# Kernel tuning notes

Measured on AMD Instinct MI355X. Metric: run time of the kernel, lower is better.

## Reference

```python
import jax, jax.numpy as jnp
import numpy as np

IMG_H, IMG_W = 800.0, 1280.0
STRIDE = 16
SCALE = 1.0 / STRIDE
P, S = 14, 1              # pooler resolution, sampling ratio
NUM_CLASSES = 80
BBOX_W = (10.0, 10.0, 5.0, 5.0)
SCORE_TH, NMS_TH, MAX_DET, IOU_TH = 0.05, 0.5, 100, 0.5
SCALE_CLAMP = float(np.log(1000.0 / 16.0))


def _make_boxes(key, n_img, n_box):
    k1, k2, k3, k4 = jax.random.split(key, 4)
    x1 = jax.random.uniform(k1, (n_img, n_box)) * (IMG_W - 64.0)
    y1 = jax.random.uniform(k2, (n_img, n_box)) * (IMG_H - 64.0)
    w = jax.random.uniform(k3, (n_img, n_box)) * 300.0 + 16.0
    h = jax.random.uniform(k4, (n_img, n_box)) * 300.0 + 16.0
    x2 = jnp.minimum(x1 + w, IMG_W)
    y2 = jnp.minimum(y1 + h, IMG_H)
    return jnp.stack([x1, y1, x2, y2], axis=-1)


def setup_inputs() -> dict:
    key = jax.random.key(0)
    ks = jax.random.split(key, 6)
    features = jax.random.normal(ks[0], (2, 50, 80, 1024), dtype=jnp.float32)
    proposals = _make_boxes(ks[1], 2, 256)
    gt_boxes = _make_boxes(ks[2], 2, 64)
    gt_classes = jax.random.randint(ks[3], (2, 64), 0, NUM_CLASSES)
    W_cls = jax.random.normal(ks[4], (1024, NUM_CLASSES + 1), dtype=jnp.float32) * 0.01
    b_cls = jnp.zeros((NUM_CLASSES + 1,), jnp.float32)
    W_box = jax.random.normal(ks[5], (1024, 4), dtype=jnp.float32) * 0.01
    b_box = jnp.zeros((4,), jnp.float32)
    return {"features": features, "proposals": proposals, "gt_boxes": gt_boxes,
            "gt_classes": gt_classes, "W_cls": W_cls, "b_cls": b_cls,
            "W_box": W_box, "b_box": b_box}


def pairwise_iou(a, b):
    # a: [G,4], b: [R,4], boxes as (x1,y1,x2,y2) -> [G,R]
    area_a = (a[:, 2] - a[:, 0]) * (a[:, 3] - a[:, 1])
    area_b = (b[:, 2] - b[:, 0]) * (b[:, 3] - b[:, 1])
    lt = jnp.maximum(a[:, None, :2], b[None, :, :2])
    rb = jnp.minimum(a[:, None, 2:], b[None, :, 2:])
    wh = jnp.clip(rb - lt, 0.0)
    inter = wh[..., 0] * wh[..., 1]
    return inter / jnp.maximum(area_a[:, None] + area_b[None, :] - inter, 1e-9)


def roi_align_one(feat, boxes):
    # feat: [H,W,C], boxes: [R,4] in image coords -> pooled [R,P,P,C]
    H, W, C = feat.shape
    b = boxes * SCALE
    x1, y1, x2, y2 = b[:, 0], b[:, 1], b[:, 2], b[:, 3]
    off = (jnp.arange(S, dtype=feat.dtype) + 0.5) / S       # [S]
    grid = jnp.arange(P, dtype=feat.dtype)                   # [P]
    bh = ((y2 - y1) / P)[:, None, None]
    bw = ((x2 - x1) / P)[:, None, None]
    # aligned RoIAlign sample coords (half-pixel offset)
    gy = y1[:, None, None] + (grid[None, :, None] + off[None, None, :]) * bh - 0.5  # [R,P,S]
    gx = x1[:, None, None] + (grid[None, :, None] + off[None, None, :]) * bw - 0.5
    gy = jnp.clip(gy, 0.0, H - 1.0)
    gx = jnp.clip(gx, 0.0, W - 1.0)
    y0 = jnp.floor(gy); x0 = jnp.floor(gx)
    y0i = y0.astype(jnp.int32); x0i = x0.astype(jnp.int32)
    y1i = jnp.minimum(y0i + 1, H - 1); x1i = jnp.minimum(x0i + 1, W - 1)
    ly = gy - y0; lx = gx - x0

    def g(yi, xi):  # cross-product gather -> [R,P,S,P,S,C]
        return feat[yi[:, :, :, None, None], xi[:, None, None, :, :]]

    wy0 = (1.0 - ly)[:, :, :, None, None, None]; wy1 = ly[:, :, :, None, None, None]
    wx0 = (1.0 - lx)[:, None, None, :, :, None]; wx1 = lx[:, None, None, :, :, None]
    val = wy0 * (wx0 * g(y0i, x0i) + wx1 * g(y0i, x1i)) \
        + wy1 * (wx0 * g(y1i, x0i) + wx1 * g(y1i, x1i))
    return val.mean(axis=(2, 4))  # average sampling points per bin -> [R,P,P,C]


def decode_boxes(deltas, boxes):
    wx, wy, ww, wh = BBOX_W
    widths = boxes[..., 2] - boxes[..., 0]
    heights = boxes[..., 3] - boxes[..., 1]
    ctr_x = boxes[..., 0] + 0.5 * widths
    ctr_y = boxes[..., 1] + 0.5 * heights
    dx = deltas[..., 0] / wx
    dy = deltas[..., 1] / wy
    dw = jnp.minimum(deltas[..., 2] / ww, SCALE_CLAMP)
    dh = jnp.minimum(deltas[..., 3] / wh, SCALE_CLAMP)
    pcx = dx * widths + ctr_x
    pcy = dy * heights + ctr_y
    pw = jnp.exp(dw) * widths
    ph = jnp.exp(dh) * heights
    out = jnp.stack([pcx - 0.5 * pw, pcy - 0.5 * ph, pcx + 0.5 * pw, pcy + 0.5 * ph], axis=-1)
    lim = jnp.array([IMG_W, IMG_H, IMG_W, IMG_H], out.dtype)
    return jnp.clip(out, 0.0, lim)


def nms_keep(boxes, scores):
    # greedy class-agnostic NMS, fixed-size keep mask [R]
    R = scores.shape[0]
    order = jnp.argsort(-scores)
    sb = boxes[order]
    iou = pairwise_iou(sb, sb)
    idx = jnp.arange(R)

    def body(i, keep):
        suppressed = jnp.any((idx < i) & keep & (iou[:, i] > NMS_TH))
        return keep.at[i].set(jnp.logical_not(suppressed))

    keep_sorted = jax.lax.fori_loop(0, R, body, jnp.ones((R,), bool))
    return jnp.zeros((R,), bool).at[order].set(keep_sorted)


def reference(features, proposals, gt_boxes, gt_classes, W_cls, b_cls, W_box, b_box):
    N, R = proposals.shape[:2]
    # --- proposal <-> gt matching (training-side labeling) ---
    iou_m = jax.vmap(pairwise_iou)(gt_boxes, proposals)          # [N,G,R]
    matched_vals = iou_m.max(axis=1)
    matched_idxs = iou_m.argmax(axis=1)                          # [N,R]
    match_labels = (matched_vals >= IOU_TH).astype(jnp.int32)    # [N,R] fg=1/bg=0
    # --- RoIAlign pooling on the single C4 feature map ---
    pooled = jax.vmap(roi_align_one)(features, proposals)        # [N,R,P,P,C]
    feat_vec = pooled.mean(axis=(2, 3))                          # res5 surrogate global avg -> [N,R,C]
    # --- box predictor ---
    scores_all = jax.nn.softmax(feat_vec @ W_cls + b_cls, axis=-1)
    fg_scores = scores_all[..., :NUM_CLASSES].max(axis=-1)       # drop background column
    deltas = feat_vec @ W_box + b_box
    boxes = decode_boxes(deltas, proposals)                      # [N,R,4]
    # --- score threshold + NMS + top-k ---
    keep = jax.vmap(nms_keep)(boxes, fg_scores) & (fg_scores > SCORE_TH)
    masked = jnp.where(keep, fg_scores, -jnp.inf)
    rank = jnp.argsort(jnp.argsort(-masked, axis=-1), axis=-1)
    keep = keep & (rank < MAX_DET)
    det = jnp.concatenate([boxes, fg_scores[..., None], keep.astype(boxes.dtype)[..., None]], axis=-1)
    return det, matched_idxs, match_labels
```

## Files before the change

kernel.cpp:

```cpp
#include <hip/hip_runtime.h>
#include <math.h>

#define N_IMG 2
#define R_PROP 256
#define G_GT 64
#define C_CH 1024
#define FH 50
#define FW 80
#define P_POOL 14
#define NCLS 80
#define IMG_W_F 1280.0f
#define IMG_H_F 800.0f
#define SCALE_F 0.0625f
#define SCORE_TH_F 0.05f
#define NMS_TH_F 0.5f
#define IOU_TH_F 0.5f
#define MAX_DET_I 100
#define SCALE_CLAMP_F 4.135166556742356f

#define NQ 4
#define QCH (C_CH / NQ)

__global__ __launch_bounds__(512) void prep_kernel(
    const float* __restrict__ proposals,
    const float* __restrict__ gt_boxes,
    int* __restrict__ perm,
    float* __restrict__ out_idx,
    float* __restrict__ out_lbl) {
  const int t = threadIdx.x;
  const int n = t >> 8;
  __shared__ float cy[N_IMG * R_PROP];
  const float* pb = proposals + (size_t)t * 4;
  float bx1 = pb[0], by1 = pb[1], bx2 = pb[2], by2 = pb[3];
  cy[t] = by1 + by2;
  __syncthreads();

  {
    float my = cy[t];
    int rk = 0;
    const int base = n * R_PROP;
#pragma unroll 8
    for (int j = base; j < base + R_PROP; ++j) {
      float cj = cy[j];
      rk += (cj < my) || (cj == my && j < t);
    }
    perm[base + rk] = t & 255;
  }

  {
    float area_b = (bx2 - bx1) * (by2 - by1);
    float best = -1.0f;
    int bidx = 0;
    const float* gt = gt_boxes + (size_t)n * G_GT * 4;
#pragma unroll 4
    for (int g = 0; g < G_GT; ++g) {
      float gx1 = gt[g * 4 + 0], gy1 = gt[g * 4 + 1];
      float gx2 = gt[g * 4 + 2], gy2 = gt[g * 4 + 3];
      float area_a = (gx2 - gx1) * (gy2 - gy1);
      float ix1 = fmaxf(gx1, bx1), iy1 = fmaxf(gy1, by1);
      float ix2 = fminf(gx2, bx2), iy2 = fminf(gy2, by2);
      float iw = fmaxf(ix2 - ix1, 0.0f), ih = fmaxf(iy2 - iy1, 0.0f);
      float inter = iw * ih;
      float iou = inter / fmaxf(area_a + area_b - inter, 1e-9f);
      if (iou > best) { best = iou; bidx = g; }
    }
    out_idx[t] = (float)bidx;
    out_lbl[t] = (best >= IOU_TH_F) ? 1.0f : 0.0f;
  }
}

__global__ __launch_bounds__(256) void roihead_kernel(
    const float* __restrict__ features,
    const float* __restrict__ proposals,
    const int* __restrict__ perm,
    const float* __restrict__ W_cls,
    const float* __restrict__ W_box,
    float* __restrict__ part) {
  const int b = blockIdx.x;
  const int xcd = b & 7;
  const int slot = b >> 3;
  const int n = xcd >> 2;
  const int band = xcd & 3;
  const int q = slot & 3;
  const int p = n * R_PROP + perm[n * R_PROP + band * 64 + (slot >> 2)];
  const int qbase = q * QCH;

  const float* feat = features + (size_t)n * (FH * FW * C_CH) + qbase;
  const int t = threadIdx.x;
  const int c4 = t & 63;
  const int g = t >> 6;

  __shared__ float s_Wy[FH];
  __shared__ float s_Wx[FW];
  __shared__ int s_b[4];
  __shared__ float4 s_red[3][64];
  __shared__ __align__(16) float sf[QCH];
  __shared__ float s_part[3][85];

  if (t < FH) s_Wy[t] = 0.0f;
  if (t >= 128 && t < 128 + FW) s_Wx[t - 128] = 0.0f;
  __syncthreads();

  if (t < 2 * P_POOL) {
    const float* pb = proposals + (size_t)p * 4;
    bool isY = t < P_POOL;
    int i = isY ? t : t - P_POOL;
    float lo = isY ? pb[1] : pb[0];
    float hi = isY ? pb[3] : pb[2];
    float limit = isY ? (float)(FH - 1) : (float)(FW - 1);
    float b1 = lo * SCALE_F, b2 = hi * SCALE_F;
    float bs = (b2 - b1) * (1.0f / P_POOL);
    float gg = b1 + ((float)i + 0.5f) * bs - 0.5f;
    gg = fminf(fmaxf(gg, 0.0f), limit);
    float fl = floorf(gg);
    int i0 = (int)fl;
    int i1 = min(i0 + 1, (int)limit);
    float l = gg - fl;
    if (isY) {
      atomicAdd(&s_Wy[i0], 1.0f - l);
      atomicAdd(&s_Wy[i1], l);
      if (i == 0) s_b[0] = i0;
      if (i == P_POOL - 1) s_b[1] = i1;
    } else {
      atomicAdd(&s_Wx[i0], 1.0f - l);
      atomicAdd(&s_Wx[i1], l);
      if (i == 0) s_b[2] = i0;
      if (i == P_POOL - 1) s_b[3] = i1;
    }
  }
  __syncthreads();

  {
    const int ylo = s_b[0], yhi = s_b[1], xlo = s_b[2], xhi = s_b[3];
    float4 acc = make_float4(0.f, 0.f, 0.f, 0.f);
    for (int y = ylo + g; y <= yhi; y += 4) {
      float wy = s_Wy[y];
      const float4* row = (const float4*)(feat + (size_t)y * (FW * C_CH)) + c4;
#pragma unroll 8
      for (int x = xlo; x <= xhi; ++x) {
        float w = wy * s_Wx[x];
        float4 f = row[x * (C_CH / 4)];
        acc.x += w * f.x;
        acc.y += w * f.y;
        acc.z += w * f.z;
        acc.w += w * f.w;
      }
    }
    if (g > 0) s_red[g - 1][c4] = acc;
    __syncthreads();
    if (g == 0) {
      const float inv = 1.0f / (float)(P_POOL * P_POOL);
#pragma unroll
      for (int r = 0; r < 3; ++r) {
        float4 a = s_red[r][c4];
        acc.x += a.x; acc.y += a.y; acc.z += a.z; acc.w += a.w;
      }
      ((float4*)sf)[c4] =
          make_float4(acc.x * inv, acc.y * inv, acc.z * inv, acc.w * inv);
    }
    __syncthreads();
  }

  {
    const int kq = t / 85;
    const int j = t - kq * 85;
    if (kq < 3) {
      float acc = 0.0f;
      if (j < 81) {
        const float* __restrict__ w = W_cls + (size_t)qbase * 81 + j;
#pragma unroll 8
        for (int k = kq; k < QCH; k += 3) acc += sf[k] * w[k * 81];
      } else {
        const float* __restrict__ w = W_box + (size_t)qbase * 4 + (j - 81);
#pragma unroll 8
        for (int k = kq; k < QCH; k += 3) acc += sf[k] * w[k * 4];
      }
      s_part[kq][j] = acc;
    }
  }
  __syncthreads();

  if (t < 85) {
    float acc = s_part[0][t] + s_part[1][t] + s_part[2][t];
    part[((size_t)p * NQ + q) * 85 + t] = acc;
  }
}

__global__ __launch_bounds__(128) void finalize_kernel(
    const float* __restrict__ part,
    const float* __restrict__ proposals,
    const float* __restrict__ b_cls,
    const float* __restrict__ b_box,
    float* __restrict__ boxes_dec,
    float* __restrict__ scores) {
  const int blk = blockIdx.x;
  const int t = threadIdx.x;
  __shared__ float sl[85];
  __shared__ float s_red[8];

  const float* pp = part + (size_t)blk * (NQ * 85);
  if (t < 85) {
    float bias = (t < 81) ? b_cls[t] : b_box[t - 81];
    sl[t] = pp[t] + pp[85 + t] + pp[170 + t] + pp[255 + t] + bias;
  }
  __syncthreads();

  {
    float xm = (t < 81) ? sl[t] : -INFINITY;
    float xf = (t < NCLS) ? sl[t] : -INFINITY;
#pragma unroll
    for (int off = 32; off; off >>= 1) {
      xm = fmaxf(xm, __shfl_down(xm, off, 64));
      xf = fmaxf(xf, __shfl_down(xf, off, 64));
    }
    if ((t & 63) == 0) { s_red[t >> 6] = xm; s_red[2 + (t >> 6)] = xf; }
  }
  __syncthreads();
  const float m = fmaxf(s_red[0], s_red[1]);
  {
    float xs = (t < 81) ? expf(sl[t] - m) : 0.0f;
#pragma unroll
    for (int off = 32; off; off >>= 1) xs += __shfl_down(xs, off, 64);
    if ((t & 63) == 0) s_red[4 + (t >> 6)] = xs;
  }
  __syncthreads();

  if (t == 0) {
    float sum = s_red[4] + s_red[5];
    float fgm = fmaxf(s_red[2], s_red[3]);
    scores[blk] = expf(fgm - m) / sum;

    const float* pb = proposals + (size_t)blk * 4;
    float w = pb[2] - pb[0], h = pb[3] - pb[1];
    float cx = pb[0] + 0.5f * w, cy = pb[1] + 0.5f * h;
    float dx = sl[81] * 0.1f;
    float dy = sl[82] * 0.1f;
    float dw = fminf(sl[83] * 0.2f, SCALE_CLAMP_F);
    float dh = fminf(sl[84] * 0.2f, SCALE_CLAMP_F);
    float pcx = dx * w + cx, pcy = dy * h + cy;
    float pw = expf(dw) * w, ph = expf(dh) * h;
    float ox1 = fminf(fmaxf(pcx - 0.5f * pw, 0.0f), IMG_W_F);
    float oy1 = fminf(fmaxf(pcy - 0.5f * ph, 0.0f), IMG_H_F);
    float ox2 = fminf(fmaxf(pcx + 0.5f * pw, 0.0f), IMG_W_F);
    float oy2 = fminf(fmaxf(pcy + 0.5f * ph, 0.0f), IMG_H_F);
    float* bd = boxes_dec + (size_t)blk * 4;
    bd[0] = ox1; bd[1] = oy1; bd[2] = ox2; bd[3] = oy2;
  }
}

__global__ __launch_bounds__(1024) void nms_kernel(
    const float* __restrict__ boxes_dec,
    const float* __restrict__ scores,
    float* __restrict__ det) {
  const int n = blockIdx.x;
  const int u = threadIdx.x;
  const int i = u & 255;
  const int q = u >> 8;
  const int j40 = q * 16;

  __shared__ __align__(16) float ss[R_PROP];
  __shared__ float4 sbs[R_PROP];
  __shared__ int s_part[4 * R_PROP];
  __shared__ int s_rank[R_PROP];
  __shared__ __align__(16) unsigned long long s_mask[R_PROP * 4];
  __shared__ unsigned long long s_keep[4];
  __shared__ __align__(16) float sm[R_PROP];

  float4 myb;
  float mys;
  if (q == 0) {
    myb = ((const float4*)boxes_dec)[n * R_PROP + i];
    mys = scores[n * R_PROP + i];
    ss[i] = mys;
  }
  __syncthreads();

  {
    float s = ss[i];
    int cnt = 0;
#pragma unroll
    for (int j4 = j40; j4 < j40 + 16; ++j4) {
      float4 v = ((const float4*)ss)[j4];
      int jb = j4 * 4;
      cnt += (v.x > s) || (v.x == s && jb + 0 < i);
      cnt += (v.y > s) || (v.y == s && jb + 1 < i);
      cnt += (v.z > s) || (v.z == s && jb + 2 < i);
      cnt += (v.w > s) || (v.w == s && jb + 3 < i);
    }
    s_part[q * R_PROP + i] = cnt;
  }
  __syncthreads();
  if (q == 0) {
    int rk = s_part[i] + s_part[R_PROP + i] + s_part[2 * R_PROP + i] +
             s_part[3 * R_PROP + i];
    s_rank[i] = rk;
    sbs[rk] = myb;
  }
  __syncthreads();

  {
    float4 bi = sbs[i];
    float area_i = (bi.z - bi.x) * (bi.w - bi.y);
    unsigned long long m = 0;
    const int j0 = q * 64;
#pragma unroll 8
    for (int jj = 0; jj < 64; ++jj) {
      float4 bj = sbs[j0 + jj];
      float area_j = (bj.z - bj.x) * (bj.w - bj.y);
      float ix1 = fmaxf(bi.x, bj.x), iy1 = fmaxf(bi.y, bj.y);
      float ix2 = fminf(bi.z, bj.z), iy2 = fminf(bi.w, bj.w);
      float iw = fmaxf(ix2 - ix1, 0.0f), ih = fmaxf(iy2 - iy1, 0.0f);
      float inter = iw * ih;
      float iou = inter / fmaxf(area_i + area_j - inter, 1e-9f);
      m |= (iou > NMS_TH_F) ? (1ull << jj) : 0ull;
    }
    s_mask[i * 4 + q] = m;
  }
  __syncthreads();

  if (u == 0) {
    unsigned long long K0 = ~0ull, K1 = ~0ull, K2 = ~0ull, K3 = ~0ull;
#pragma unroll 16
    for (int b = 1; b < 64; ++b) {
      unsigned long long m0 = s_mask[(size_t)b * 4 + 0];
      unsigned long long sup = m0 & K0 & ((1ull << b) - 1ull);
      K0 = sup ? (K0 & ~(1ull << b)) : K0;
    }
#pragma unroll 16
    for (int b = 0; b < 64; ++b) {
      const unsigned long long* mi = &s_mask[(size_t)(64 + b) * 4];
      unsigned long long m0 = mi[0], m1 = mi[1];
      unsigned long long sup = (m0 & K0) | (m1 & K1 & ((1ull << b) - 1ull));
      K1 = sup ? (K1 & ~(1ull << b)) : K1;
    }
#pragma unroll 16
    for (int b = 0; b < 64; ++b) {
      const unsigned long long* mi = &s_mask[(size_t)(128 + b) * 4];
      unsigned long long m0 = mi[0], m1 = mi[1], m2 = mi[2];
      unsigned long long sup =
          (m0 & K0) | (m1 & K1) | (m2 & K2 & ((1ull << b) - 1ull));
      K2 = sup ? (K2 & ~(1ull << b)) : K2;
    }
#pragma unroll 16
    for (int b = 0; b < 64; ++b) {
      const unsigned long long* mi = &s_mask[(size_t)(192 + b) * 4];
      unsigned long long m0 = mi[0], m1 = mi[1], m2 = mi[2], m3 = mi[3];
      unsigned long long sup = (m0 & K0) | (m1 & K1) | (m2 & K2) |
                               (m3 & K3 & ((1ull << b) - 1ull));
      K3 = sup ? (K3 & ~(1ull << b)) : K3;
    }
    s_keep[0] = K0; s_keep[1] = K1; s_keep[2] = K2; s_keep[3] = K3;
  }
  __syncthreads();

  bool kept = false;
  if (q == 0) {
    int rk = s_rank[i];
    kept = ((s_keep[rk >> 6] >> (rk & 63)) & 1ull) && (mys > SCORE_TH_F);
    sm[i] = kept ? mys : -INFINITY;
  }
  __syncthreads();

  {
    float mym = sm[i];
    int cnt = 0;
#pragma unroll
    for (int j4 = j40; j4 < j40 + 16; ++j4) {
      float4 v = ((const float4*)sm)[j4];
      int jb = j4 * 4;
      cnt += (v.x > mym) || (v.x == mym && jb + 0 < i);
      cnt += (v.y > mym) || (v.y == mym && jb + 1 < i);
      cnt += (v.z > mym) || (v.z == mym && jb + 2 < i);
      cnt += (v.w > mym) || (v.w == mym && jb + 3 < i);
    }
    s_part[q * R_PROP + i] = cnt;
  }
  __syncthreads();

  if (q == 0) {
    int rk2 = s_part[i] + s_part[R_PROP + i] + s_part[2 * R_PROP + i] +
              s_part[3 * R_PROP + i];
    kept = kept && (rk2 < MAX_DET_I);
    float* dr = det + ((size_t)n * R_PROP + i) * 6;
    dr[0] = myb.x; dr[1] = myb.y; dr[2] = myb.z; dr[3] = myb.w;
    dr[4] = mys;
    dr[5] = kept ? 1.0f : 0.0f;
  }
}

extern "C" void kernel_launch(void* const* d_in, const int* in_sizes, int n_in,
                              void* d_out, int out_size, void* d_ws, size_t ws_size,
                              hipStream_t stream) {
  const float* features  = (const float*)d_in[0];
  const float* proposals = (const float*)d_in[1];
  const float* gt_boxes  = (const float*)d_in[2];
  const float* W_cls = (const float*)d_in[4];
  const float* b_cls = (const float*)d_in[5];
  const float* W_box = (const float*)d_in[6];
  const float* b_box = (const float*)d_in[7];

  float* out = (float*)d_out;
  float* out_det = out;
  float* out_idx = out + N_IMG * R_PROP * 6;
  float* out_lbl = out_idx + N_IMG * R_PROP;

  int*   perm      = (int*)d_ws;
  float* part      = (float*)(perm + 512);
  float* boxes_dec = part + (size_t)N_IMG * R_PROP * NQ * 85;
  float* scores    = boxes_dec + (size_t)N_IMG * R_PROP * 4;

  prep_kernel<<<1, 512, 0, stream>>>(proposals, gt_boxes, perm, out_idx,
                                     out_lbl);
  roihead_kernel<<<N_IMG * R_PROP * NQ, 256, 0, stream>>>(
      features, proposals, perm, W_cls, W_box, part);
  finalize_kernel<<<N_IMG * R_PROP, 128, 0, stream>>>(
      part, proposals, b_cls, b_box, boxes_dec, scores);
  nms_kernel<<<N_IMG, 1024, 0, stream>>>(boxes_dec, scores, out_det);
}
```

Baseline: 163.8 us.

## Fuse finalize and NMS into RoI kernel via last-block atomic counters

Merges the finalize and NMS kernels into the RoI pooling kernel. Atomic completion counters pick a single block to run each later stage: the last of the four channel-quarter blocks per proposal reduces the partial sums and decodes its box, and the last proposal block per image runs NMS with 256 threads. The prep kernel now runs one block per image and resets the counters. This removes two kernel launches and their gaps, but the NMS tail now runs on fewer threads with a serial dependency, and it adds threadfence and atomic overhead.

```diff
diff --git a/kernel.cpp b/kernel.cpp
--- a/kernel.cpp
+++ b/kernel.cpp
@@ -21,30 +21,35 @@
 #define NQ 4
 #define QCH (C_CH / NQ)
 
-__global__ __launch_bounds__(512) void prep_kernel(
+__global__ __launch_bounds__(256) void prep_kernel(
     const float* __restrict__ proposals,
     const float* __restrict__ gt_boxes,
     int* __restrict__ perm,
+    int* __restrict__ qdone,
+    int* __restrict__ idone,
     float* __restrict__ out_idx,
     float* __restrict__ out_lbl) {
+  const int n = blockIdx.x;
   const int t = threadIdx.x;
-  const int n = t >> 8;
-  __shared__ float cy[N_IMG * R_PROP];
-  const float* pb = proposals + (size_t)t * 4;
+  const int gid = n * R_PROP + t;
+  __shared__ float cy[R_PROP];
+
+  const float* pb = proposals + (size_t)gid * 4;
   float bx1 = pb[0], by1 = pb[1], bx2 = pb[2], by2 = pb[3];
   cy[t] = by1 + by2;
+  qdone[gid] = 0;
+  if (t == 0) idone[n] = 0;
   __syncthreads();
 
   {
     float my = cy[t];
     int rk = 0;
-    const int base = n * R_PROP;
-#pragma unroll 8
-    for (int j = base; j < base + R_PROP; ++j) {
+#pragma unroll 8
+    for (int j = 0; j < R_PROP; ++j) {
       float cj = cy[j];
       rk += (cj < my) || (cj == my && j < t);
     }
-    perm[base + rk] = t & 255;
+    perm[n * R_PROP + rk] = t;
   }
 
   {
@@ -64,18 +69,48 @@
       float iou = inter / fmaxf(area_a + area_b - inter, 1e-9f);
       if (iou > best) { best = iou; bidx = g; }
     }
-    out_idx[t] = (float)bidx;
-    out_lbl[t] = (best >= IOU_TH_F) ? 1.0f : 0.0f;
+    out_idx[gid] = (float)bidx;
+    out_lbl[gid] = (best >= IOU_TH_F) ? 1.0f : 0.0f;
   }
 }
 
-__global__ __launch_bounds__(256) void roihead_kernel(
+__global__ __launch_bounds__(256, 8) void mega_kernel(
     const float* __restrict__ features,
     const float* __restrict__ proposals,
     const int* __restrict__ perm,
     const float* __restrict__ W_cls,
     const float* __restrict__ W_box,
-    float* __restrict__ part) {
+    const float* __restrict__ b_cls,
+    const float* __restrict__ b_box,
+    float* __restrict__ part,
+    float* __restrict__ boxes_dec,
+    float* __restrict__ scores,
+    int* __restrict__ qdone,
+    int* __restrict__ idone,
+    float* __restrict__ det) {
+  union SMem {
+    struct {
+      float Wy[FH];
+      float Wx[FW];
+      int bb[4];
+      float4 red[3][64];
+      float sf[QCH];
+      float part3[3][85];
+      float sl[85];
+      float red2[8];
+    } roi;
+    struct {
+      float ss[R_PROP];
+      float4 sbs[R_PROP];
+      int rank[R_PROP];
+      unsigned long long mask[R_PROP * 4];
+      unsigned long long keep[4];
+      float sm[R_PROP];
+    } nms;
+  };
+  __shared__ __align__(16) SMem u;
+  __shared__ int s_flag;
+
   const int b = blockIdx.x;
   const int xcd = b & 7;
   const int slot = b >> 3;
@@ -90,15 +125,8 @@
   const int c4 = t & 63;
   const int g = t >> 6;
 
-  __shared__ float s_Wy[FH];
-  __shared__ float s_Wx[FW];
-  __shared__ int s_b[4];
-  __shared__ float4 s_red[3][64];
-  __shared__ __align__(16) float sf[QCH];
-  __shared__ float s_part[3][85];
-
-  if (t < FH) s_Wy[t] = 0.0f;
-  if (t >= 128 && t < 128 + FW) s_Wx[t - 128] = 0.0f;
+  if (t < FH) u.roi.Wy[t] = 0.0f;
+  if (t >= 128 && t < 128 + FW) u.roi.Wx[t - 128] = 0.0f;
   __syncthreads();
 
   if (t < 2 * P_POOL) {
@@ -117,28 +145,29 @@
     int i1 = min(i0 + 1, (int)limit);
     float l = gg - fl;
     if (isY) {
-      atomicAdd(&s_Wy[i0], 1.0f - l);
-      atomicAdd(&s_Wy[i1], l);
-      if (i == 0) s_b[0] = i0;
-      if (i == P_POOL - 1) s_b[1] = i1;
+      atomicAdd(&u.roi.Wy[i0], 1.0f - l);
+      atomicAdd(&u.roi.Wy[i1], l);
+      if (i == 0) u.roi.bb[0] = i0;
+      if (i == P_POOL - 1) u.roi.bb[1] = i1;
     } else {
-      atomicAdd(&s_Wx[i0], 1.0f - l);
-      atomicAdd(&s_Wx[i1], l);
-      if (i == 0) s_b[2] = i0;
-      if (i == P_POOL - 1) s_b[3] = i1;
-    }
-  }
-  __syncthreads();
-
-  {
-    const int ylo = s_b[0], yhi = s_b[1], xlo = s_b[2], xhi = s_b[3];
+      atomicAdd(&u.roi.Wx[i0], 1.0f - l);
+      atomicAdd(&u.roi.Wx[i1], l);
+      if (i == 0) u.roi.bb[2] = i0;
+      if (i == P_POOL - 1) u.roi.bb[3] = i1;
+    }
+  }
+  __syncthreads();
+
+  {
+    const int ylo = u.roi.bb[0], yhi = u.roi.bb[1];
+    const int xlo = u.roi.bb[2], xhi = u.roi.bb[3];
     float4 acc = make_float4(0.f, 0.f, 0.f, 0.f);
     for (int y = ylo + g; y <= yhi; y += 4) {
-      float wy = s_Wy[y];
+      float wy = u.roi.Wy[y];
       const float4* row = (const float4*)(feat + (size_t)y * (FW * C_CH)) + c4;
 #pragma unroll 8
       for (int x = xlo; x <= xhi; ++x) {
-        float w = wy * s_Wx[x];
+        float w = wy * u.roi.Wx[x];
         float4 f = row[x * (C_CH / 4)];
         acc.x += w * f.x;
         acc.y += w * f.y;
@@ -146,16 +175,16 @@
         acc.w += w * f.w;
       }
     }
-    if (g > 0) s_red[g - 1][c4] = acc;
+    if (g > 0) u.roi.red[g - 1][c4] = acc;
     __syncthreads();
     if (g == 0) {
       const float inv = 1.0f / (float)(P_POOL * P_POOL);
 #pragma unroll
       for (int r = 0; r < 3; ++r) {
-        float4 a = s_red[r][c4];
+        float4 a = u.roi.red[r][c4];
         acc.x += a.x; acc.y += a.y; acc.z += a.z; acc.w += a.w;
       }
-      ((float4*)sf)[c4] =
+      ((float4*)u.roi.sf)[c4] =
           make_float4(acc.x * inv, acc.y * inv, acc.z * inv, acc.w * inv);
     }
     __syncthreads();
@@ -169,218 +198,197 @@
       if (j < 81) {
         const float* __restrict__ w = W_cls + (size_t)qbase * 81 + j;
 #pragma unroll 8
-        for (int k = kq; k < QCH; k += 3) acc += sf[k] * w[k * 81];
+        for (int k = kq; k < QCH; k += 3) acc += u.roi.sf[k] * w[k * 81];
       } else {
         const float* __restrict__ w = W_box + (size_t)qbase * 4 + (j - 81);
 #pragma unroll 8
-        for (int k = kq; k < QCH; k += 3) acc += sf[k] * w[k * 4];
+        for (int k = kq; k < QCH; k += 3) acc += u.roi.sf[k] * w[k * 4];
       }
-      s_part[kq][j] = acc;
+      u.roi.part3[kq][j] = acc;
     }
   }
   __syncthreads();
 
   if (t < 85) {
-    float acc = s_part[0][t] + s_part[1][t] + s_part[2][t];
+    float acc = u.roi.part3[0][t] + u.roi.part3[1][t] + u.roi.part3[2][t];
     part[((size_t)p * NQ + q) * 85 + t] = acc;
   }
-}
-
-__global__ __launch_bounds__(128) void finalize_kernel(
-    const float* __restrict__ part,
-    const float* __restrict__ proposals,
-    const float* __restrict__ b_cls,
-    const float* __restrict__ b_box,
-    float* __restrict__ boxes_dec,
-    float* __restrict__ scores) {
-  const int blk = blockIdx.x;
-  const int t = threadIdx.x;
-  __shared__ float sl[85];
-  __shared__ float s_red[8];
-
-  const float* pp = part + (size_t)blk * (NQ * 85);
-  if (t < 85) {
-    float bias = (t < 81) ? b_cls[t] : b_box[t - 81];
-    sl[t] = pp[t] + pp[85 + t] + pp[170 + t] + pp[255 + t] + bias;
-  }
-  __syncthreads();
-
-  {
-    float xm = (t < 81) ? sl[t] : -INFINITY;
-    float xf = (t < NCLS) ? sl[t] : -INFINITY;
+
+  __syncthreads();
+  if (t == 0) {
+    __threadfence();
+    s_flag = (atomicAdd(&qdone[p], 1) == NQ - 1) ? 1 : 0;
+  }
+  __syncthreads();
+  if (!s_flag) return;
+  __threadfence();
+
+  {
+    const float* pp = part + (size_t)p * (NQ * 85);
+    if (t < 85) {
+      float bias = (t < 81) ? b_cls[t] : b_box[t - 81];
+      u.roi.sl[t] = pp[t] + pp[85 + t] + pp[170 + t] + pp[255 + t] + bias;
+    }
+  }
+  __syncthreads();
+
+  if (t < 128) {
+    float xm = (t < 81) ? u.roi.sl[t] : -INFINITY;
+    float xf = (t < NCLS) ? u.roi.sl[t] : -INFINITY;
 #pragma unroll
     for (int off = 32; off; off >>= 1) {
       xm = fmaxf(xm, __shfl_down(xm, off, 64));
       xf = fmaxf(xf, __shfl_down(xf, off, 64));
     }
-    if ((t & 63) == 0) { s_red[t >> 6] = xm; s_red[2 + (t >> 6)] = xf; }
-  }
-  __syncthreads();
-  const float m = fmaxf(s_red[0], s_red[1]);
-  {
-    float xs = (t < 81) ? expf(sl[t] - m) : 0.0f;
+    if ((t & 63) == 0) { u.roi.red2[t >> 6] = xm; u.roi.red2[2 + (t >> 6)] = xf; }
+  }
+  __syncthreads();
+  if (t < 128) {
+    const float m = fmaxf(u.roi.red2[0], u.roi.red2[1]);
+    float xs = (t < 81) ? expf(u.roi.sl[t] - m) : 0.0f;
 #pragma unroll
     for (int off = 32; off; off >>= 1) xs += __shfl_down(xs, off, 64);
-    if ((t & 63) == 0) s_red[4 + (t >> 6)] = xs;
+    if ((t & 63) == 0) u.roi.red2[4 + (t >> 6)] = xs;
   }
   __syncthreads();
 
   if (t == 0) {
-    float sum = s_red[4] + s_red[5];
-    float fgm = fmaxf(s_red[2], s_red[3]);
-    scores[blk] = expf(fgm - m) / sum;
-
-    const float* pb = proposals + (size_t)blk * 4;
+    const float m = fmaxf(u.roi.red2[0], u.roi.red2[1]);
+    float sum = u.roi.red2[4] + u.roi.red2[5];
+    float fgm = fmaxf(u.roi.red2[2], u.roi.red2[3]);
+    scores[p] = expf(fgm - m) / sum;
+
+    const float* pb = proposals + (size_t)p * 4;
     float w = pb[2] - pb[0], h = pb[3] - pb[1];
     float cx = pb[0] + 0.5f * w, cy = pb[1] + 0.5f * h;
-    float dx = sl[81] * 0.1f;
-    float dy = sl[82] * 0.1f;
-    float dw = fminf(sl[83] * 0.2f, SCALE_CLAMP_F);
-    float dh = fminf(sl[84] * 0.2f, SCALE_CLAMP_F);
+    float dx = u.roi.sl[81] * 0.1f;
+    float dy = u.roi.sl[82] * 0.1f;
+    float dw = fminf(u.roi.sl[83] * 0.2f, SCALE_CLAMP_F);
+    float dh = fminf(u.roi.sl[84] * 0.2f, SCALE_CLAMP_F);
     float pcx = dx * w + cx, pcy = dy * h + cy;
     float pw = expf(dw) * w, ph = expf(dh) * h;
     float ox1 = fminf(fmaxf(pcx - 0.5f * pw, 0.0f), IMG_W_F);
     float oy1 = fminf(fmaxf(pcy - 0.5f * ph, 0.0f), IMG_H_F);
     float ox2 = fminf(fmaxf(pcx + 0.5f * pw, 0.0f), IMG_W_F);
     float oy2 = fminf(fmaxf(pcy + 0.5f * ph, 0.0f), IMG_H_F);
-    float* bd = boxes_dec + (size_t)blk * 4;
+    float* bd = boxes_dec + (size_t)p * 4;
     bd[0] = ox1; bd[1] = oy1; bd[2] = ox2; bd[3] = oy2;
   }
-}
-
-__global__ __launch_bounds__(1024) void nms_kernel(
-    const float* __restrict__ boxes_dec,
-    const float* __restrict__ scores,
-    float* __restrict__ det) {
-  const int n = blockIdx.x;
-  const int u = threadIdx.x;
-  const int i = u & 255;
-  const int q = u >> 8;
-  const int j40 = q * 16;
-
-  __shared__ __align__(16) float ss[R_PROP];
-  __shared__ float4 sbs[R_PROP];
-  __shared__ int s_part[4 * R_PROP];
-  __shared__ int s_rank[R_PROP];
-  __shared__ __align__(16) unsigned long long s_mask[R_PROP * 4];
-  __shared__ unsigned long long s_keep[4];
-  __shared__ __align__(16) float sm[R_PROP];
-
-  float4 myb;
-  float mys;
-  if (q == 0) {
-    myb = ((const float4*)boxes_dec)[n * R_PROP + i];
-    mys = scores[n * R_PROP + i];
-    ss[i] = mys;
-  }
-  __syncthreads();
-
-  {
-    float s = ss[i];
+
+  __syncthreads();
+  if (t == 0) {
+    __threadfence();
+    s_flag = (atomicAdd(&idone[n], 1) == R_PROP - 1) ? 1 : 0;
+  }
+  __syncthreads();
+  if (!s_flag) return;
+  __threadfence();
+
+  const int i = t;
+  float4 myb = ((const float4*)boxes_dec)[n * R_PROP + i];
+  float mys = scores[n * R_PROP + i];
+  u.nms.ss[i] = mys;
+  __syncthreads();
+
+  {
+    float s = u.nms.ss[i];
     int cnt = 0;
-#pragma unroll
-    for (int j4 = j40; j4 < j40 + 16; ++j4) {
-      float4 v = ((const float4*)ss)[j4];
+#pragma unroll 8
+    for (int j4 = 0; j4 < 64; ++j4) {
+      float4 v = ((const float4*)u.nms.ss)[j4];
       int jb = j4 * 4;
       cnt += (v.x > s) || (v.x == s && jb + 0 < i);
       cnt += (v.y > s) || (v.y == s && jb + 1 < i);
       cnt += (v.z > s) || (v.z == s && jb + 2 < i);
       cnt += (v.w > s) || (v.w == s && jb + 3 < i);
     }
-    s_part[q * R_PROP + i] = cnt;
-  }
-  __syncthreads();
-  if (q == 0) {
-    int rk = s_part[i] + s_part[R_PROP + i] + s_part[2 * R_PROP + i] +
-             s_part[3 * R_PROP + i];
-    s_rank[i] = rk;
-    sbs[rk] = myb;
-  }
-  __syncthreads();
-
-  {
-    float4 bi = sbs[i];
+    u.nms.rank[i] = cnt;
+    u.nms.sbs[cnt] = myb;
+  }
+  __syncthreads();
+
+  {
+    float4 bi = u.nms.sbs[i];
     float area_i = (bi.z - bi.x) * (bi.w - bi.y);
-    unsigned long long m = 0;
-    const int j0 = q * 64;
-#pragma unroll 8
-    for (int jj = 0; jj < 64; ++jj) {
-      float4 bj = sbs[j0 + jj];
-      float area_j = (bj.z - bj.x) * (bj.w - bj.y);
-      float ix1 = fmaxf(bi.x, bj.x), iy1 = fmaxf(bi.y, bj.y);
-      float ix2 = fminf(bi.z, bj.z), iy2 = fminf(bi.w, bj.w);
-      float iw = fmaxf(ix2 - ix1, 0.0f), ih = fmaxf(iy2 - iy1, 0.0f);
-      float inter = iw * ih;
-      float iou = inter / fmaxf(area_i + area_j - inter, 1e-9f);
-      m |= (iou > NMS_TH_F) ? (1ull << jj) : 0ull;
-    }
-    s_mask[i * 4 + q] = m;
-  }
-  __syncthreads();
-
-  if (u == 0) {
+#pragma unroll
+    for (int qq = 0; qq < 4; ++qq) {
+      unsigned long long m = 0;
+      const int j0 = qq * 64;
+#pragma unroll 8
+      for (int jj = 0; jj < 64; ++jj) {
+        float4 bj = u.nms.sbs[j0 + jj];
+        float area_j = (bj.z - bj.x) * (bj.w - bj.y);
+        float ix1 = fmaxf(bi.x, bj.x), iy1 = fmaxf(bi.y, bj.y);
+        float ix2 = fminf(bi.z, bj.z), iy2 = fminf(bi.w, bj.w);
+        float iw = fmaxf(ix2 - ix1, 0.0f), ih = fmaxf(iy2 - iy1, 0.0f);
+        float inter = iw * ih;
+        float iou = inter / fmaxf(area_i + area_j - inter, 1e-9f);
+        m |= (iou > NMS_TH_F) ? (1ull << jj) : 0ull;
+      }
+      u.nms.mask[i * 4 + qq] = m;
+    }
+  }
+  __syncthreads();
+
+  if (t == 0) {
     unsigned long long K0 = ~0ull, K1 = ~0ull, K2 = ~0ull, K3 = ~0ull;
 #pragma unroll 16
-    for (int b = 1; b < 64; ++b) {
-      unsigned long long m0 = s_mask[(size_t)b * 4 + 0];
-      unsigned long long sup = m0 & K0 & ((1ull << b) - 1ull);
-      K0 = sup ? (K0 & ~(1ull << b)) : K0;
+    for (int bb = 1; bb < 64; ++bb) {
+      unsigned long long m0 = u.nms.mask[(size_t)bb * 4 + 0];
+      unsigned long long sup = m0 & K0 & ((1ull << bb) - 1ull);
+      K0 = sup ? (K0 & ~(1ull << bb)) : K0;
     }
 #pragma unroll 16
-    for (int b = 0; b < 64; ++b) {
-      const unsigned long long* mi = &s_mask[(size_t)(64 + b) * 4];
+    for (int bb = 0; bb < 64; ++bb) {
+      const unsigned long long* mi = &u.nms.mask[(size_t)(64 + bb) * 4];
       unsigned long long m0 = mi[0], m1 = mi[1];
-      unsigned long long sup = (m0 & K0) | (m1 & K1 & ((1ull << b) - 1ull));
-      K1 = sup ? (K1 & ~(1ull << b)) : K1;
+      unsigned long long sup = (m0 & K0) | (m1 & K1 & ((1ull << bb) - 1ull));
+      K1 = sup ? (K1 & ~(1ull << bb)) : K1;
     }
 #pragma unroll 16
-    for (int b = 0; b < 64; ++b) {
-      const unsigned long long* mi = &s_mask[(size_t)(128 + b) * 4];
+    for (int bb = 0; bb < 64; ++bb) {
+      const unsigned long long* mi = &u.nms.mask[(size_t)(128 + bb) * 4];
       unsigned long long m0 = mi[0], m1 = mi[1], m2 = mi[2];
       unsigned long long sup =
-          (m0 & K0) | (m1 & K1) | (m2 & K2 & ((1ull << b) - 1ull));
-      K2 = sup ? (K2 & ~(1ull << b)) : K2;
+          (m0 & K0) | (m1 & K1) | (m2 & K2 & ((1ull << bb) - 1ull));
+      K2 = sup ? (K2 & ~(1ull << bb)) : K2;
     }
 #pragma unroll 16
-    for (int b = 0; b < 64; ++b) {
-      const unsigned long long* mi = &s_mask[(size_t)(192 + b) * 4];
+    for (int bb = 0; bb < 64; ++bb) {
+      const unsigned long long* mi = &u.nms.mask[(size_t)(192 + bb) * 4];
       unsigned long long m0 = mi[0], m1 = mi[1], m2 = mi[2], m3 = mi[3];
       unsigned long long sup = (m0 & K0) | (m1 & K1) | (m2 & K2) |
-                               (m3 & K3 & ((1ull << b) - 1ull));
-      K3 = sup ? (K3 & ~(1ull << b)) : K3;
-    }
-    s_keep[0] = K0; s_keep[1] = K1; s_keep[2] = K2; s_keep[3] = K3;
-  }
-  __syncthreads();
-
-  bool kept = false;
-  if (q == 0) {
-    int rk = s_rank[i];
-    kept = ((s_keep[rk >> 6] >> (rk & 63)) & 1ull) && (mys > SCORE_TH_F);
-    sm[i] = kept ? mys : -INFINITY;
-  }
-  __syncthreads();
-
-  {
-    float mym = sm[i];
+                               (m3 & K3 & ((1ull << bb) - 1ull));
+      K3 = sup ? (K3 & ~(1ull << bb)) : K3;
+    }
+    u.nms.keep[0] = K0; u.nms.keep[1] = K1;
+    u.nms.keep[2] = K2; u.nms.keep[3] = K3;
+  }
+  __syncthreads();
+
+  bool kept;
+  {
+    int rk = u.nms.rank[i];
+    kept = ((u.nms.keep[rk >> 6] >> (rk & 63)) & 1ull) && (mys > SCORE_TH_F);
+    u.nms.sm[i] = kept ? mys : -INFINITY;
+  }
+  __syncthreads();
+
+  {
+    float mym = u.nms.sm[i];
     int cnt = 0;
-#pragma unroll
-    for (int j4 = j40; j4 < j40 + 16; ++j4) {
-      float4 v = ((const float4*)sm)[j4];
+#pragma unroll 8
+    for (int j4 = 0; j4 < 64; ++j4) {
+      float4 v = ((const float4*)u.nms.sm)[j4];
       int jb = j4 * 4;
       cnt += (v.x > mym) || (v.x == mym && jb + 0 < i);
       cnt += (v.y > mym) || (v.y == mym && jb + 1 < i);
       cnt += (v.z > mym) || (v.z == mym && jb + 2 < i);
       cnt += (v.w > mym) || (v.w == mym && jb + 3 < i);
     }
-    s_part[q * R_PROP + i] = cnt;
-  }
-  __syncthreads();
-
-  if (q == 0) {
-    int rk2 = s_part[i] + s_part[R_PROP + i] + s_part[2 * R_PROP + i] +
-              s_part[3 * R_PROP + i];
-    kept = kept && (rk2 < MAX_DET_I);
+    kept = kept && (cnt < MAX_DET_I);
+  }
+  {
     float* dr = det + ((size_t)n * R_PROP + i) * 6;
     dr[0] = myb.x; dr[1] = myb.y; dr[2] = myb.z; dr[3] = myb.w;
     dr[4] = mys;
@@ -405,15 +413,15 @@
   float* out_lbl = out_idx + N_IMG * R_PROP;
 
   int*   perm      = (int*)d_ws;
-  float* part      = (float*)(perm + 512);
+  int*   qdone     = perm + 512;
+  int*   idone     = qdone + 512;
+  float* part      = (float*)(idone + 16);
   float* boxes_dec = part + (size_t)N_IMG * R_PROP * NQ * 85;
   float* scores    = boxes_dec + (size_t)N_IMG * R_PROP * 4;
 
-  prep_kernel<<<1, 512, 0, stream>>>(proposals, gt_boxes, perm, out_idx,
-                                     out_lbl);
-  roihead_kernel<<<N_IMG * R_PROP * NQ, 256, 0, stream>>>(
-      features, proposals, perm, W_cls, W_box, part);
-  finalize_kernel<<<N_IMG * R_PROP, 128, 0, stream>>>(
-      part, proposals, b_cls, b_box, boxes_dec, scores);
-  nms_kernel<<<N_IMG, 1024, 0, stream>>>(boxes_dec, scores, out_det);
+  prep_kernel<<<N_IMG, 256, 0, stream>>>(proposals, gt_boxes, perm, qdone,
+                                         idone, out_idx, out_lbl);
+  mega_kernel<<<N_IMG * R_PROP * NQ, 256, 0, stream>>>(
+      features, proposals, perm, W_cls, W_box, b_cls, b_box, part, boxes_dec,
+      scores, qdone, idone, out_det);
 }
```

Measured after the change: 264.5 us. +61.5%, slower.
